# Kernel tuning notes

Measured on AMD Instinct MI355X. Metric: run time of the kernel, lower is better.

## Reference

```python
import jax, jax.numpy as jnp
import numpy as np

NEG_MASK_SCALE = -1e-09  # faithful to source (source uses -1e-09, likely intended -1e9)


def setup_inputs() -> dict:
    key0 = jax.random.key(0)
    ks = jax.random.split(key0, 7)
    B, Q, K, H = 4, 256, 1024, 128
    return {
        "query": jax.random.normal(ks[0], (B, Q, H), dtype=jnp.float32),
        "key": jax.random.normal(ks[1], (B, K, H), dtype=jnp.float32),
        "value": jax.random.normal(ks[2], (B, K, H), dtype=jnp.float32),
        "mask": jax.random.randint(ks[3], (B, Q, K), 0, 2).astype(jnp.int32),
        "Wq": jax.random.normal(ks[4], (H, H), dtype=jnp.float32) * (1.0 / np.sqrt(H)),
        "Wk": jax.random.normal(ks[5], (H, H), dtype=jnp.float32) * (1.0 / np.sqrt(H)),
        "v": jax.random.normal(ks[6], (H,), dtype=jnp.float32) * (1.0 / np.sqrt(H)),
    }


def reference(query, key, value, mask, Wq, Wk, v):
    # Projections: torch Linear computes x @ W.T
    q_proj = jnp.einsum("bqd,hd->bqh", query, Wq)  # (B, Q, H)
    k_proj = jnp.einsum("bkd,hd->bkh", key, Wk)    # (B, K, H)
    # Additive (Bahdanau) score: v . tanh(q_proj[:, :, None] + k_proj[:, None])
    feat = jnp.tanh(q_proj[:, :, None, :] + k_proj[:, None, :, :])  # (B, Q, K, H)
    score = jnp.einsum("bqkh,h->bqk", feat, v)                      # (B, Q, K)
    score = score + NEG_MASK_SCALE * (1.0 - mask.astype(score.dtype))
    attention_weights = jax.nn.softmax(score, axis=-1)              # (B, Q, K)
    context_vector = jnp.einsum("bqk,bkv->bqv", attention_weights, value)  # (B, Q, V)
    return attention_weights, context_vector
```

## Files before the change

kernel.cpp:

```cpp
#include <hip/hip_runtime.h>

#define Bb 4
#define Qn 256
#define Kn 1024
#define Hn 128
#define QT 4

constexpr float SCALE = 2.88539008177792681f;

#if __has_builtin(__builtin_amdgcn_exp2f)
#define EXP2F(x) __builtin_amdgcn_exp2f(x)
#else
#define EXP2F(x) exp2f(x)
#endif
#if __has_builtin(__builtin_amdgcn_rcpf)
#define RCPF(x) __builtin_amdgcn_rcpf(x)
#else
#define RCPF(x) (1.0f / (x))
#endif

__global__ __launch_bounds__(128) void proj_kernel(const float* __restrict__ query,
                                                   const float* __restrict__ key,
                                                   const float* __restrict__ Wq,
                                                   const float* __restrict__ Wk,
                                                   float* __restrict__ eqT,
                                                   float* __restrict__ ekT) {
    __shared__ float4 xs[128];
    const int tid = threadIdx.x;
    const bool isQ = blockIdx.x < (Bb * Qn / 4);
    const int r0 = (isQ ? blockIdx.x : blockIdx.x - Bb * Qn / 4) * 4;
    const float* x = isQ ? query : key;
    const float* W = isQ ? Wq : Wk;

    xs[tid] = ((const float4*)(x + (size_t)r0 * Hn))[tid];
    __syncthreads();
    const float4* W4 = (const float4*)W + (size_t)tid * (Hn / 4);
    float acc0 = 0.f, acc1 = 0.f, acc2 = 0.f, acc3 = 0.f;
#pragma unroll 8
    for (int d = 0; d < Hn / 4; ++d) {
        float4 w = W4[d];
        float4 a0 = xs[d];
        float4 a1 = xs[32 + d];
        float4 a2 = xs[64 + d];
        float4 a3 = xs[96 + d];
        acc0 = fmaf(w.x, a0.x, fmaf(w.y, a0.y, fmaf(w.z, a0.z, fmaf(w.w, a0.w, acc0))));
        acc1 = fmaf(w.x, a1.x, fmaf(w.y, a1.y, fmaf(w.z, a1.z, fmaf(w.w, a1.w, acc1))));
        acc2 = fmaf(w.x, a2.x, fmaf(w.y, a2.y, fmaf(w.z, a2.z, fmaf(w.w, a2.w, acc2))));
        acc3 = fmaf(w.x, a3.x, fmaf(w.y, a3.y, fmaf(w.z, a3.z, fmaf(w.w, a3.w, acc3))));
    }
    float4 res = make_float4(EXP2F(acc0 * SCALE), EXP2F(acc1 * SCALE),
                             EXP2F(acc2 * SCALE), EXP2F(acc3 * SCALE));
    if (isQ) {
        const int b = r0 / Qn;
        const int q0 = r0 % Qn;
        ((float4*)eqT)[((size_t)b * Hn + tid) * (Qn / 4) + (q0 >> 2)] = res;
    } else {
        const int b = r0 / Kn;
        const int k0 = r0 % Kn;
        ((float4*)ekT)[((size_t)b * Hn + tid) * (Kn / 4) + (k0 >> 2)] = res;
    }
}

__global__ __launch_bounds__(1024) void fused_attn_kernel(const float* __restrict__ eqT,
                                                          const float* __restrict__ ekT,
                                                          const float* __restrict__ v,
                                                          const float* __restrict__ value,
                                                          float* __restrict__ attn,
                                                          float* __restrict__ ctx) {
    const int tid = threadIdx.x;
    const int q0 = blockIdx.x * QT;
    const int b = blockIdx.y;

    __shared__ __align__(16) float sc[QT][Kn];
    __shared__ float red[16][QT];
    __shared__ __align__(16) float4 pl[8][QT][Hn / 4];

    const int k = tid;
    const float4* eqb = (const float4*)(eqT + (size_t)b * Hn * Qn) + (q0 >> 2);
    const float* ekb = ekT + (size_t)b * Hn * Kn + k;
    float a0 = 0.f, a1 = 0.f, a2 = 0.f, a3 = 0.f;
#pragma unroll 8
    for (int h = 0; h < Hn; ++h) {
        const float4 qv = eqb[(size_t)h * (Qn / 4)];
        const float vh = v[h];
        const float kv = ekb[(size_t)h * Kn];
        float r;
        r = RCPF(fmaf(qv.x, kv, 1.0f)); a0 = fmaf(vh, r, a0);
        r = RCPF(fmaf(qv.y, kv, 1.0f)); a1 = fmaf(vh, r, a1);
        r = RCPF(fmaf(qv.z, kv, 1.0f)); a2 = fmaf(vh, r, a2);
        r = RCPF(fmaf(qv.w, kv, 1.0f)); a3 = fmaf(vh, r, a3);
    }

    const int lane = tid & 63, wv = tid >> 6;
    float m0 = a0, m1 = a1, m2 = a2, m3 = a3;
#pragma unroll
    for (int off = 32; off; off >>= 1) {
        m0 = fminf(m0, __shfl_xor(m0, off));
        m1 = fminf(m1, __shfl_xor(m1, off));
        m2 = fminf(m2, __shfl_xor(m2, off));
        m3 = fminf(m3, __shfl_xor(m3, off));
    }
    if (lane == 0) {
        red[wv][0] = m0; red[wv][1] = m1; red[wv][2] = m2; red[wv][3] = m3;
    }
    __syncthreads();
    m0 = red[0][0]; m1 = red[0][1]; m2 = red[0][2]; m3 = red[0][3];
#pragma unroll
    for (int w = 1; w < 16; ++w) {
        m0 = fminf(m0, red[w][0]); m1 = fminf(m1, red[w][1]);
        m2 = fminf(m2, red[w][2]); m3 = fminf(m3, red[w][3]);
    }
    __syncthreads();

    float e0 = EXP2F((m0 - a0) * SCALE);
    float e1 = EXP2F((m1 - a1) * SCALE);
    float e2 = EXP2F((m2 - a2) * SCALE);
    float e3 = EXP2F((m3 - a3) * SCALE);
    float s0 = e0, s1 = e1, s2 = e2, s3 = e3;
#pragma unroll
    for (int off = 32; off; off >>= 1) {
        s0 += __shfl_xor(s0, off);
        s1 += __shfl_xor(s1, off);
        s2 += __shfl_xor(s2, off);
        s3 += __shfl_xor(s3, off);
    }
    if (lane == 0) {
        red[wv][0] = s0; red[wv][1] = s1; red[wv][2] = s2; red[wv][3] = s3;
    }
    __syncthreads();
    s0 = red[0][0]; s1 = red[0][1]; s2 = red[0][2]; s3 = red[0][3];
#pragma unroll
    for (int w = 1; w < 16; ++w) {
        s0 += red[w][0]; s1 += red[w][1]; s2 += red[w][2]; s3 += red[w][3];
    }

    const float w0 = e0 * RCPF(s0);
    const float w1 = e1 * RCPF(s1);
    const float w2 = e2 * RCPF(s2);
    const float w3 = e3 * RCPF(s3);
    sc[0][k] = w0; sc[1][k] = w1; sc[2][k] = w2; sc[3][k] = w3;
    float* arow = attn + ((size_t)b * Qn + q0) * Kn + k;
    arow[0 * Kn] = w0; arow[1 * Kn] = w1; arow[2 * Kn] = w2; arow[3 * Kn] = w3;
    __syncthreads();

    const int kc = tid >> 7;
    const int cq = (tid >> 5) & 3;
    const int h4 = tid & 31;
    const float4* vb = (const float4*)(value + ((size_t)b * Kn + kc * 128) * Hn) + h4;
    const float* wr = &sc[cq][kc * 128];
    float4 acc = make_float4(0.f, 0.f, 0.f, 0.f);
#pragma unroll 4
    for (int kk = 0; kk < 128; ++kk) {
        const float wgt = wr[kk];
        const float4 vv = vb[(size_t)kk * (Hn / 4)];
        acc.x = fmaf(wgt, vv.x, acc.x);
        acc.y = fmaf(wgt, vv.y, acc.y);
        acc.z = fmaf(wgt, vv.z, acc.z);
        acc.w = fmaf(wgt, vv.w, acc.w);
    }
    pl[kc][cq][h4] = acc;
    __syncthreads();
    if (tid < QT * Hn / 4) {
        const int q = tid >> 5, h = tid & 31;
        float4 r0 = pl[0][q][h], r1 = pl[1][q][h], r2 = pl[2][q][h], r3 = pl[3][q][h];
        float4 r4 = pl[4][q][h], r5 = pl[5][q][h], r6 = pl[6][q][h], r7 = pl[7][q][h];
        float4 sum;
        sum.x = ((r0.x + r1.x) + (r2.x + r3.x)) + ((r4.x + r5.x) + (r6.x + r7.x));
        sum.y = ((r0.y + r1.y) + (r2.y + r3.y)) + ((r4.y + r5.y) + (r6.y + r7.y));
        sum.z = ((r0.z + r1.z) + (r2.z + r3.z)) + ((r4.z + r5.z) + (r6.z + r7.z));
        sum.w = ((r0.w + r1.w) + (r2.w + r3.w)) + ((r4.w + r5.w) + (r6.w + r7.w));
        ((float4*)(ctx + ((size_t)b * Qn + q0 + q) * Hn))[h] = sum;
    }
}

extern "C" void kernel_launch(void* const* d_in, const int* in_sizes, int n_in,
                              void* d_out, int out_size, void* d_ws, size_t ws_size,
                              hipStream_t stream) {
    const float* query = (const float*)d_in[0];
    const float* key = (const float*)d_in[1];
    const float* value = (const float*)d_in[2];
    const float* Wq = (const float*)d_in[4];
    const float* Wk = (const float*)d_in[5];
    const float* v = (const float*)d_in[6];

    float* out = (float*)d_out;
    float* attn = out;
    float* ctx = out + (size_t)Bb * Qn * Kn;

    float* ws = (float*)d_ws;
    float* eqT = ws;
    float* ekT = ws + 131072;

    proj_kernel<<<dim3(Bb * Qn / 4 + Bb * Kn / 4), dim3(128), 0, stream>>>(
        query, key, Wq, Wk, eqT, ekT);
    fused_attn_kernel<<<dim3(Qn / QT, Bb), dim3(1024), 0, stream>>>(
        eqT, ekT, v, value, attn, ctx);
}
```

Before: 119.0 us.

## Remap score threads to one query per wave group with float4 keys and prefetch

The score phase now gives each thread four consecutive keys for a single query instead of one key across four queries. The query exponential becomes a wave-uniform scalar load and key loads become float4, software-prefetched eight rows ahead in registers. This halves the per-query reduction work, because each query's min and sum now combine over 4 waves rather than 16, and it lets the attention row be stored as float4. The cost is more registers for the prefetch buffer, which could reduce occupancy.

Measured after the change: 118.1 us. About the same (-0.8%).

```diff
diff --git a/kernel.cpp b/kernel.cpp
--- a/kernel.cpp
+++ b/kernel.cpp
@@ -5,6 +5,7 @@
 #define Kn 1024
 #define Hn 128
 #define QT 4
+#define PF 8
 
 constexpr float SCALE = 2.88539008177792681f;
 
@@ -72,75 +73,60 @@
     const int b = blockIdx.y;
 
     __shared__ __align__(16) float sc[QT][Kn];
-    __shared__ float red[16][QT];
+    __shared__ float red[16][2];
     __shared__ __align__(16) float4 pl[8][QT][Hn / 4];
 
-    const int k = tid;
-    const float4* eqb = (const float4*)(eqT + (size_t)b * Hn * Qn) + (q0 >> 2);
-    const float* ekb = ekT + (size_t)b * Hn * Kn + k;
+    const int kg = tid & 255;
+    const int qu = __builtin_amdgcn_readfirstlane(tid >> 8);
+    const float4* ekp = (const float4*)(ekT + (size_t)b * Hn * Kn) + kg;
+    const float* eqs = eqT + (size_t)b * Hn * Qn + q0 + qu;
+
+    float4 pf[PF];
+#pragma unroll
+    for (int j = 0; j < PF; ++j) pf[j] = ekp[(size_t)j * (Kn / 4)];
+
     float a0 = 0.f, a1 = 0.f, a2 = 0.f, a3 = 0.f;
-#pragma unroll 8
-    for (int h = 0; h < Hn; ++h) {
-        const float4 qv = eqb[(size_t)h * (Qn / 4)];
-        const float vh = v[h];
-        const float kv = ekb[(size_t)h * Kn];
-        float r;
-        r = RCPF(fmaf(qv.x, kv, 1.0f)); a0 = fmaf(vh, r, a0);
-        r = RCPF(fmaf(qv.y, kv, 1.0f)); a1 = fmaf(vh, r, a1);
-        r = RCPF(fmaf(qv.z, kv, 1.0f)); a2 = fmaf(vh, r, a2);
-        r = RCPF(fmaf(qv.w, kv, 1.0f)); a3 = fmaf(vh, r, a3);
+    for (int c = 0; c < Hn / PF; ++c) {
+#pragma unroll
+        for (int j = 0; j < PF; ++j) {
+            const int h = c * PF + j;
+            const float4 kv = pf[j];
+            if (c < Hn / PF - 1) pf[j] = ekp[(size_t)(h + PF) * (Kn / 4)];
+            const float qe = eqs[(size_t)h * Qn];
+            const float vh = v[h];
+            float r;
+            r = RCPF(fmaf(qe, kv.x, 1.0f)); a0 = fmaf(vh, r, a0);
+            r = RCPF(fmaf(qe, kv.y, 1.0f)); a1 = fmaf(vh, r, a1);
+            r = RCPF(fmaf(qe, kv.z, 1.0f)); a2 = fmaf(vh, r, a2);
+            r = RCPF(fmaf(qe, kv.w, 1.0f)); a3 = fmaf(vh, r, a3);
+        }
     }
 
     const int lane = tid & 63, wv = tid >> 6;
-    float m0 = a0, m1 = a1, m2 = a2, m3 = a3;
+    float mn = fminf(fminf(a0, a1), fminf(a2, a3));
 #pragma unroll
-    for (int off = 32; off; off >>= 1) {
-        m0 = fminf(m0, __shfl_xor(m0, off));
-        m1 = fminf(m1, __shfl_xor(m1, off));
-        m2 = fminf(m2, __shfl_xor(m2, off));
-        m3 = fminf(m3, __shfl_xor(m3, off));
-    }
-    if (lane == 0) {
-        red[wv][0] = m0; red[wv][1] = m1; red[wv][2] = m2; red[wv][3] = m3;
-    }
+    for (int off = 32; off; off >>= 1) mn = fminf(mn, __shfl_xor(mn, off));
+    if (lane == 0) red[wv][0] = mn;
     __syncthreads();
-    m0 = red[0][0]; m1 = red[0][1]; m2 = red[0][2]; m3 = red[0][3];
+    mn = fminf(fminf(red[qu * 4][0], red[qu * 4 + 1][0]),
+               fminf(red[qu * 4 + 2][0], red[qu * 4 + 3][0]));
+
+    const float e0 = EXP2F((mn - a0) * SCALE);
+    const float e1 = EXP2F((mn - a1) * SCALE);
+    const float e2 = EXP2F((mn - a2) * SCALE);
+    const float e3 = EXP2F((mn - a3) * SCALE);
+    float s = (e0 + e1) + (e2 + e3);
 #pragma unroll
-    for (int w = 1; w < 16; ++w) {
-        m0 = fminf(m0, red[w][0]); m1 = fminf(m1, red[w][1]);
-        m2 = fminf(m2, red[w][2]); m3 = fminf(m3, red[w][3]);
-    }
+    for (int off = 32; off; off >>= 1) s += __shfl_xor(s, off);
+    if (lane == 0) red[wv][1] = s;
     __syncthreads();
+    s = (red[qu * 4][1] + red[qu * 4 + 1][1]) +
+        (red[qu * 4 + 2][1] + red[qu * 4 + 3][1]);
+    const float inv = RCPF(s);
 
-    float e0 = EXP2F((m0 - a0) * SCALE);
-    float e1 = EXP2F((m1 - a1) * SCALE);
-    float e2 = EXP2F((m2 - a2) * SCALE);
-    float e3 = EXP2F((m3 - a3) * SCALE);
-    float s0 = e0, s1 = e1, s2 = e2, s3 = e3;
-#pragma unroll
-    for (int off = 32; off; off >>= 1) {
-        s0 += __shfl_xor(s0, off);
-        s1 += __shfl_xor(s1, off);
-        s2 += __shfl_xor(s2, off);
-        s3 += __shfl_xor(s3, off);
-    }
-    if (lane == 0) {
-        red[wv][0] = s0; red[wv][1] = s1; red[wv][2] = s2; red[wv][3] = s3;
-    }
-    __syncthreads();
-    s0 = red[0][0]; s1 = red[0][1]; s2 = red[0][2]; s3 = red[0][3];
-#pragma unroll
-    for (int w = 1; w < 16; ++w) {
-        s0 += red[w][0]; s1 += red[w][1]; s2 += red[w][2]; s3 += red[w][3];
-    }
-
-    const float w0 = e0 * RCPF(s0);
-    const float w1 = e1 * RCPF(s1);
-    const float w2 = e2 * RCPF(s2);
-    const float w3 = e3 * RCPF(s3);
-    sc[0][k] = w0; sc[1][k] = w1; sc[2][k] = w2; sc[3][k] = w3;
-    float* arow = attn + ((size_t)b * Qn + q0) * Kn + k;
-    arow[0 * Kn] = w0; arow[1 * Kn] = w1; arow[2 * Kn] = w2; arow[3 * Kn] = w3;
+    const float4 w4 = make_float4(e0 * inv, e1 * inv, e2 * inv, e3 * inv);
+    ((float4*)&sc[qu][0])[kg] = w4;
+    ((float4*)(attn + ((size_t)b * Qn + q0 + qu) * Kn))[kg] = w4;
     __syncthreads();
 
     const int kc = tid >> 7;
```
